# Kernel tuning notes

Measured on AMD Instinct MI355X. Metric: run time of the kernel, lower is better.

## Reference

```python
import jax, jax.numpy as jnp
import numpy as np

N = 131072          # total sampled proposals (flattened over batch)
D = 1024            # num_extractor_out
C = 21              # num_classes (VOC: 20 + background)


def setup_inputs() -> dict:
    key = jax.random.key(0)
    k1, k2, k3 = jax.random.split(key, 3)
    features = jax.random.normal(k1, (N, D), dtype=jnp.float32)
    # Linear weights stored as [in, out] so y = x @ W + b
    W_cls = jax.random.normal(k2, (D, C), dtype=jnp.float32) * (1.0 / np.sqrt(D))
    b_cls = jnp.zeros((C,), dtype=jnp.float32)
    W_tf = jax.random.normal(k3, (D, C * 4), dtype=jnp.float32) * (1.0 / np.sqrt(D))
    b_tf = jnp.zeros((C * 4,), dtype=jnp.float32)
    return {"features": features, "W_cls": W_cls, "b_cls": b_cls, "W_tf": W_tf, "b_tf": b_tf}


def reference(features, W_cls, b_cls, W_tf, b_tf):
    # ROI.forward with identity extractor / no pre/post transforms.
    proposal_classes = features @ W_cls + b_cls                    # [N, C]
    proposal_transformers = features @ W_tf + b_tf                 # [N, C*4]
    proposal_transformers = proposal_transformers.reshape(features.shape[0], C, 4)
    return proposal_classes, proposal_transformers
```

## Files before the change

kernel.cpp:

```cpp
#include <hip/hip_runtime.h>
#include <hip/hip_bf16.h>

#define NROWS 131072
#define DK    1024
#define CCLS  21
#define CTF   84
#define NCOL  105
#define NCT   7
#define BM    128
#define BKF   64
#define NSLAB (DK / BKF)

typedef __attribute__((ext_vector_type(4))) float f32x4;
typedef __attribute__((ext_vector_type(8))) short bf16x8;

typedef const __attribute__((address_space(1))) void GV;
typedef __attribute__((address_space(3))) void LV;

__device__ __forceinline__ unsigned short f2bf_rne(float x) {
    union { float f; unsigned u; } v; v.f = x;
    unsigned r = v.u + 0x7fffu + ((v.u >> 16) & 1u);
    return (unsigned short)(r >> 16);
}

__device__ __forceinline__ unsigned pack2(float lo, float hi) {
    union { float f; unsigned u; } a, b; a.f = lo; b.f = hi;
    return ((a.u + 0x8000u) >> 16) | ((b.u + 0x8000u) & 0xffff0000u);
}

__device__ __forceinline__ bf16x8 cvt8v(const f32x4 lo, const f32x4 hi) {
    union { unsigned u[4]; bf16x8 v; } r;
    r.u[0] = pack2(lo[0], lo[1]);
    r.u[1] = pack2(lo[2], lo[3]);
    r.u[2] = pack2(hi[0], hi[1]);
    r.u[3] = pack2(hi[2], hi[3]);
    return r.v;
}

__global__ void pack_B_kernel(const float* __restrict__ Wc,
                              const float* __restrict__ Wt,
                              unsigned short* __restrict__ Bp) {
    const int frag = blockIdx.x;
    const int kt = frag / NCT, ct = frag % NCT;
    const int lane = threadIdx.x;
    const int col = ct * 16 + (lane & 15);
    const int k0  = kt * 32 + ((lane >> 4) << 3);
    bf16x8 o;
#pragma unroll
    for (int j = 0; j < 8; ++j) {
        const int k = k0 + j;
        float v = 0.0f;
        if (col < CCLS)      v = Wc[k * CCLS + col];
        else if (col < NCOL) v = Wt[k * CTF + (col - CCLS)];
        o[j] = (short)f2bf_rne(v);
    }
    *reinterpret_cast<bf16x8*>(Bp + ((size_t)frag * 64 + lane) * 8) = o;
}

__global__ __launch_bounds__(256, 2)
void roi_gemm_kernel(const float* __restrict__ F,
                     const unsigned short* __restrict__ Bp,
                     const float* __restrict__ bcls,
                     const float* __restrict__ btf,
                     float* __restrict__ out) {
    __shared__ float Alds[2][4][32][BKF];

    const int t    = threadIdx.x;
    const int wave = t >> 6;
    const int lane = t & 63;
    const int fr   = lane & 15;
    const int fq   = lane >> 4;
    const int sw   = fr & 7;

    const long rw = (long)blockIdx.x * BM + wave * 32;

    const float* srcE = F + (size_t)(rw + fq) * DK + ((fr ^ fq) << 2);
    const float* srcO = F + (size_t)(rw + fq) * DK + ((fr ^ (fq + 4)) << 2);
    const unsigned short* bb = Bp + (size_t)lane * 8;

    f32x4 acc[2][NCT];
#pragma unroll
    for (int a = 0; a < 2; ++a)
#pragma unroll
        for (int b = 0; b < NCT; ++b)
            acc[a][b] = (f32x4){0.f, 0.f, 0.f, 0.f};

#define STAGE(BUF, S) do {                                                   \
    const float* _e = srcE + (size_t)(S) * BKF;                              \
    const float* _o = srcO + (size_t)(S) * BKF;                              \
    _Pragma("unroll")                                                        \
    for (int q = 0; q < 8; ++q) {                                            \
        const float* g = ((q & 1) ? _o : _e) + (size_t)q * 4 * DK;           \
        __builtin_amdgcn_global_load_lds((GV*)g,                             \
            (LV*)&Alds[BUF][wave][q * 4][0], 16, 0, 0);                      \
    }                                                                        \
} while (0)

    STAGE(0, 0);

    for (int s = 0; s < NSLAB; ++s) {
        const int buf = s & 1;

        __builtin_amdgcn_sched_barrier(0);
        bf16x8 bf[2][NCT];
#pragma unroll
        for (int kt = 0; kt < 2; ++kt)
#pragma unroll
            for (int ct = 0; ct < NCT; ++ct)
                bf[kt][ct] = *reinterpret_cast<const bf16x8*>(
                    bb + ((size_t)((s * 2 + kt) * NCT + ct) * 512));
        __builtin_amdgcn_sched_barrier(0);

        if (s + 1 < NSLAB) {
            STAGE((s + 1) & 1, s + 1);
            __builtin_amdgcn_sched_barrier(0);
            asm volatile("s_waitcnt vmcnt(8)" ::: "memory");
        } else {
            asm volatile("s_waitcnt vmcnt(0)" ::: "memory");
        }
        __builtin_amdgcn_sched_barrier(0);

#pragma unroll
        for (int kt = 0; kt < 2; ++kt) {
            bf16x8 af[2];
#pragma unroll
            for (int rt = 0; rt < 2; ++rt) {
                const float* lpr = &Alds[buf][wave][rt * 16 + fr][0];
                const int c0 = kt * 8 + fq * 2;
                const f32x4 lo = *reinterpret_cast<const f32x4*>(
                    lpr + (((c0 + 0) ^ sw) << 2));
                const f32x4 hi = *reinterpret_cast<const f32x4*>(
                    lpr + (((c0 + 1) ^ sw) << 2));
                af[rt] = cvt8v(lo, hi);
            }
#pragma unroll
            for (int ct = 0; ct < NCT; ++ct) {
                acc[0][ct] = __builtin_amdgcn_mfma_f32_16x16x32_bf16(
                    af[0], bf[kt][ct], acc[0][ct], 0, 0, 0);
                acc[1][ct] = __builtin_amdgcn_mfma_f32_16x16x32_bf16(
                    af[1], bf[kt][ct], acc[1][ct], 0, 0, 0);
            }
        }
    }
#undef STAGE

    float* out_tf = out + (size_t)NROWS * CCLS;
#pragma unroll
    for (int rt = 0; rt < 2; ++rt) {
        const long rbase = rw + rt * 16 + (fq << 2);
#pragma unroll
        for (int ct = 0; ct < NCT; ++ct) {
            const int col = ct * 16 + fr;
            if (col >= NCOL) continue;
            const float bias = (col < CCLS) ? bcls[col] : btf[col - CCLS];
#pragma unroll
            for (int j = 0; j < 4; ++j) {
                const long row = rbase + j;
                const float v = acc[rt][ct][j] + bias;
                if (col < CCLS) out[row * CCLS + col] = v;
                else            out_tf[row * CTF + (col - CCLS)] = v;
            }
        }
    }
}

extern "C" void kernel_launch(void* const* d_in, const int* in_sizes, int n_in,
                              void* d_out, int out_size, void* d_ws, size_t ws_size,
                              hipStream_t stream) {
    const float* F  = (const float*)d_in[0];
    const float* Wc = (const float*)d_in[1];
    const float* bc = (const float*)d_in[2];
    const float* Wt = (const float*)d_in[3];
    const float* bt = (const float*)d_in[4];
    unsigned short* Bp = (unsigned short*)d_ws;

    pack_B_kernel<<<NCT * (DK / 32), 64, 0, stream>>>(Wc, Wt, Bp);
    roi_gemm_kernel<<<NROWS / BM, 256, 0, stream>>>(F, Bp, bc, bt, (float*)d_out);
}
```

Baseline: 153.3 us.

## Shrink per-wave tile to 16 rows with deeper 256-wide K slabs

Each wave now computes 16 rows instead of 32, blocks shrink to 128 threads covering 32 rows, and each staged K slab grows from 64 to 256 floats with 16 async LDS loads per stage. B fragments are loaded per k-step inside the inner loop rather than up front per slab. The goal is more blocks in flight and longer prefetch runs to hide memory latency on this bandwidth-bound GEMM. In exchange, B fragment reuse per wave is halved, so B traffic from L2 doubles.

```diff
diff --git a/kernel.cpp b/kernel.cpp
--- a/kernel.cpp
+++ b/kernel.cpp
@@ -7,9 +7,10 @@
 #define CTF   84
 #define NCOL  105
 #define NCT   7
-#define BM    128
-#define BKF   64
-#define NSLAB (DK / BKF)
+#define WROWS 16
+#define SLABF 256
+#define NSLAB (DK / SLABF)
+#define KTPS  (SLABF / 32)
 
 typedef __attribute__((ext_vector_type(4))) float f32x4;
 typedef __attribute__((ext_vector_type(8))) short bf16x8;
@@ -57,13 +58,13 @@
     *reinterpret_cast<bf16x8*>(Bp + ((size_t)frag * 64 + lane) * 8) = o;
 }
 
-__global__ __launch_bounds__(256, 2)
+__global__ __launch_bounds__(128)
 void roi_gemm_kernel(const float* __restrict__ F,
                      const unsigned short* __restrict__ Bp,
                      const float* __restrict__ bcls,
                      const float* __restrict__ btf,
                      float* __restrict__ out) {
-    __shared__ float Alds[2][4][32][BKF];
+    __shared__ float Alds[2][2][WROWS][SLABF];
 
     const int t    = threadIdx.x;
     const int wave = t >> 6;
@@ -72,28 +73,27 @@
     const int fq   = lane >> 4;
     const int sw   = fr & 7;
 
-    const long rw = (long)blockIdx.x * BM + wave * 32;
+    const long rww = (long)blockIdx.x * (2 * WROWS) + wave * WROWS;
 
-    const float* srcE = F + (size_t)(rw + fq) * DK + ((fr ^ fq) << 2);
-    const float* srcO = F + (size_t)(rw + fq) * DK + ((fr ^ (fq + 4)) << 2);
+    const float* p[8];
+#pragma unroll
+    for (int j = 0; j < 8; ++j)
+        p[j] = F + (size_t)(rww + j) * DK + ((lane ^ j) << 2);
+
     const unsigned short* bb = Bp + (size_t)lane * 8;
 
-    f32x4 acc[2][NCT];
+    f32x4 acc[NCT];
 #pragma unroll
-    for (int a = 0; a < 2; ++a)
-#pragma unroll
-        for (int b = 0; b < NCT; ++b)
-            acc[a][b] = (f32x4){0.f, 0.f, 0.f, 0.f};
+    for (int b = 0; b < NCT; ++b) acc[b] = (f32x4){0.f, 0.f, 0.f, 0.f};
 
-#define STAGE(BUF, S) do {                                                   \
-    const float* _e = srcE + (size_t)(S) * BKF;                              \
-    const float* _o = srcO + (size_t)(S) * BKF;                              \
-    _Pragma("unroll")                                                        \
-    for (int q = 0; q < 8; ++q) {                                            \
-        const float* g = ((q & 1) ? _o : _e) + (size_t)q * 4 * DK;           \
-        __builtin_amdgcn_global_load_lds((GV*)g,                             \
-            (LV*)&Alds[BUF][wave][q * 4][0], 16, 0, 0);                      \
-    }                                                                        \
+#define STAGE(BUF, S) do {                                                    \
+    _Pragma("unroll")                                                         \
+    for (int q = 0; q < 16; ++q) {                                            \
+        const float* g = p[q & 7] + ((q >> 3) ? (size_t)8 * DK : (size_t)0)   \
+                         + (size_t)(S) * SLABF;                               \
+        __builtin_amdgcn_global_load_lds((GV*)g,                              \
+            (LV*)&Alds[wave][BUF][q][0], 16, 0, 0);                           \
+    }                                                                         \
 } while (0)
 
     STAGE(0, 0);
@@ -102,64 +102,51 @@
         const int buf = s & 1;
 
         __builtin_amdgcn_sched_barrier(0);
-        bf16x8 bf[2][NCT];
-#pragma unroll
-        for (int kt = 0; kt < 2; ++kt)
-#pragma unroll
-            for (int ct = 0; ct < NCT; ++ct)
-                bf[kt][ct] = *reinterpret_cast<const bf16x8*>(
-                    bb + ((size_t)((s * 2 + kt) * NCT + ct) * 512));
-        __builtin_amdgcn_sched_barrier(0);
-
         if (s + 1 < NSLAB) {
-            STAGE((s + 1) & 1, s + 1);
+            STAGE(buf ^ 1, s + 1);
             __builtin_amdgcn_sched_barrier(0);
-            asm volatile("s_waitcnt vmcnt(8)" ::: "memory");
+            asm volatile("s_waitcnt vmcnt(16)" ::: "memory");
         } else {
             asm volatile("s_waitcnt vmcnt(0)" ::: "memory");
         }
         __builtin_amdgcn_sched_barrier(0);
 
+        const float* lpr = &Alds[wave][buf][fr][0];
 #pragma unroll
-        for (int kt = 0; kt < 2; ++kt) {
-            bf16x8 af[2];
+        for (int kt = 0; kt < KTPS; ++kt) {
+            const int gkt = s * KTPS + kt;
+            bf16x8 bf[NCT];
 #pragma unroll
-            for (int rt = 0; rt < 2; ++rt) {
-                const float* lpr = &Alds[buf][wave][rt * 16 + fr][0];
-                const int c0 = kt * 8 + fq * 2;
-                const f32x4 lo = *reinterpret_cast<const f32x4*>(
-                    lpr + (((c0 + 0) ^ sw) << 2));
-                const f32x4 hi = *reinterpret_cast<const f32x4*>(
-                    lpr + (((c0 + 1) ^ sw) << 2));
-                af[rt] = cvt8v(lo, hi);
-            }
+            for (int ct = 0; ct < NCT; ++ct)
+                bf[ct] = *reinterpret_cast<const bf16x8*>(
+                    bb + ((size_t)(gkt * NCT + ct) * 512));
+            const int c0 = kt * 8 + fq * 2;
+            const f32x4 lo = *reinterpret_cast<const f32x4*>(
+                lpr + (((c0 + 0) ^ sw) << 2));
+            const f32x4 hi = *reinterpret_cast<const f32x4*>(
+                lpr + (((c0 + 1) ^ sw) << 2));
+            const bf16x8 af = cvt8v(lo, hi);
 #pragma unroll
-            for (int ct = 0; ct < NCT; ++ct) {
-                acc[0][ct] = __builtin_amdgcn_mfma_f32_16x16x32_bf16(
-                    af[0], bf[kt][ct], acc[0][ct], 0, 0, 0);
-                acc[1][ct] = __builtin_amdgcn_mfma_f32_16x16x32_bf16(
-                    af[1], bf[kt][ct], acc[1][ct], 0, 0, 0);
-            }
+            for (int ct = 0; ct < NCT; ++ct)
+                acc[ct] = __builtin_amdgcn_mfma_f32_16x16x32_bf16(
+                    af, bf[ct], acc[ct], 0, 0, 0);
         }
     }
 #undef STAGE
 
     float* out_tf = out + (size_t)NROWS * CCLS;
+    const long rbase = rww + (fq << 2);
 #pragma unroll
-    for (int rt = 0; rt < 2; ++rt) {
-        const long rbase = rw + rt * 16 + (fq << 2);
+    for (int ct = 0; ct < NCT; ++ct) {
+        const int col = ct * 16 + fr;
+        if (col >= NCOL) continue;
+        const float bias = (col < CCLS) ? bcls[col] : btf[col - CCLS];
 #pragma unroll
-        for (int ct = 0; ct < NCT; ++ct) {
-            const int col = ct * 16 + fr;
-            if (col >= NCOL) continue;
-            const float bias = (col < CCLS) ? bcls[col] : btf[col - CCLS];
-#pragma unroll
-            for (int j = 0; j < 4; ++j) {
-                const long row = rbase + j;
-                const float v = acc[rt][ct][j] + bias;
-                if (col < CCLS) out[row * CCLS + col] = v;
-                else            out_tf[row * CTF + (col - CCLS)] = v;
-            }
+        for (int j = 0; j < 4; ++j) {
+            const long row = rbase + j;
+            const float v = acc[ct][j] + bias;
+            if (col < CCLS) out[row * CCLS + col] = v;
+            else            out_tf[row * CTF + (col - CCLS)] = v;
         }
     }
 }
@@ -175,5 +162,6 @@
     unsigned short* Bp = (unsigned short*)d_ws;
 
     pack_B_kernel<<<NCT * (DK / 32), 64, 0, stream>>>(Wc, Wt, Bp);
-    roi_gemm_kernel<<<NROWS / BM, 256, 0, stream>>>(F, Bp, bc, bt, (float*)d_out);
+    roi_gemm_kernel<<<NROWS / (2 * WROWS), 128, 0, stream>>>(F, Bp, bc, bt,
+                                                             (float*)d_out);
 }
```

New measurement: 212.5 us. 38.6% more time.
